# Kernel optimization log

Measured on AMD Instinct MI355X. Metric: run time of the kernel, lower is better.

The kernel has to match this reference:

```python
import jax, jax.numpy as jnp
import numpy as np

B, C, L, H, W = 2, 64, 8, 32, 32

def setup_inputs() -> dict:
    key = jax.random.key(0)
    ks = jax.random.split(key, 10)
    return {
        "q": jax.random.normal(ks[0], (B, C, L, H, W), dtype=jnp.float32),
        "k": jax.random.normal(ks[1], (B, C, L, H, W), dtype=jnp.float32),
        "v": jax.random.normal(ks[2], (B, C, L, H, W), dtype=jnp.float32),
        "wq": jax.random.normal(ks[3], (C,), dtype=jnp.float32) * 0.1,
        "bq": jax.random.normal(ks[4], (1,), dtype=jnp.float32) * 0.1,
        "wk": jax.random.normal(ks[5], (C,), dtype=jnp.float32) * 0.1,
        "bk": jax.random.normal(ks[6], (1,), dtype=jnp.float32) * 0.1,
        "wv": jax.random.normal(ks[7], (C, 3 * C), dtype=jnp.float32) * 0.1,
        "bv": jax.random.normal(ks[8], (C,), dtype=jnp.float32) * 0.1,
        "gamma_x": jax.random.normal(ks[9], (1,), dtype=jnp.float32) * 0.1,
    }


def reference(q, k, v, wq, bq, wk, bk, wv, bv, gamma_x):
    # q,k,v: [B,C,L,H,W]; 1x1x1 conv3d == channel contraction
    Bq, Cq, Lq, Hq, Wq = q.shape
    N = Lq * Hq * Wq
    qf = q.reshape(Bq, Cq, N)
    kf = k.reshape(Bq, Cq, N)
    vf = v.reshape(Bq, Cq, N)
    # query/key conv: C -> 1 channel => [B, N]
    pq = jnp.einsum('bcn,c->bn', qf, wq) + bq  # [B,N]
    pk = jnp.einsum('bcn,c->bn', kf, wk) + bk  # [B,N]
    # energy = bmm([B,N,1],[B,1,N]) = outer product -> [B,N,N]
    energy = pq[:, :, None] * pk[:, None, :]
    attn = jax.nn.softmax(energy, axis=-1)  # softmax over key index n
    # value path: cat(v, q, k) along channels -> [B,3C,N], then 3C -> C conv
    val = jnp.concatenate([vf, qf, kf], axis=1)
    pv = jnp.einsum('bdn,cd->bcn', val, wv) + bv[None, :, None]  # [B,C,N]
    # out[b,c,m] = sum_n pv[b,c,n] * attn[b,m,n]  (bmm with attn^T)
    out = jnp.einsum('bcn,bmn->bcm', pv, attn).reshape(Bq, Cq, Lq, Hq, Wq)
    return gamma_x * out + v
```

## Files before the change

### kernel.cpp

```cpp
#include <hip/hip_runtime.h>


typedef __attribute__((ext_vector_type(8))) __bf16 bf16x8;
typedef __attribute__((ext_vector_type(4))) float  f32x4;

#define NN 8192
#define CC 64
#define NJ 48

__global__ __launch_bounds__(256) void fused_kernel(
    const float* __restrict__ q, const float* __restrict__ k,
    const float* __restrict__ v,
    const float* __restrict__ wq, const float* __restrict__ bq,
    const float* __restrict__ wk, const float* __restrict__ bk,
    const float* __restrict__ wv, const float* __restrict__ bv,
    float* __restrict__ pq, float* __restrict__ G, float* __restrict__ T)
{
    __shared__ __align__(16) __bf16 val_sT[64][200];
    __shared__ __align__(16) __bf16 pv_s[64][72];
    __shared__ __align__(16) __bf16 V_s[NJ][72];
    __shared__ float pq4[4][64], pk4[4][64];

    int t = threadIdx.x, lane = t & 63, wid = t >> 6;
    int quad = lane >> 4, cl = lane & 15;
    int b  = blockIdx.x >> 7;
    int n0 = (blockIdx.x & 127) << 6;
    size_t bo = (size_t)b * CC * NN;

    bf16x8 wvA[6];
    const float* wr = wv + (size_t)(wid * 16 + cl) * 192;
    #pragma unroll
    for (int ks = 0; ks < 6; ks++) {
        f32x4 a0 = *(const f32x4*)(wr + ks * 32 + quad * 8);
        f32x4 a1 = *(const f32x4*)(wr + ks * 32 + quad * 8 + 4);
        #pragma unroll
        for (int e = 0; e < 4; e++) {
            wvA[ks][e]     = (__bf16)a0[e];
            wvA[ks][4 + e] = (__bf16)a1[e];
        }
    }
    float bvr[4];
    #pragma unroll
    for (int r = 0; r < 4; r++) bvr[r] = bv[wid * 16 + quad * 4 + r];

    {
        const float* qp = q + bo + (size_t)(wid * 16) * NN + n0 + lane;
        const float* kp = k + bo + (size_t)(wid * 16) * NN + n0 + lane;
        float aq = 0.f, ak = 0.f;
        #pragma unroll
        for (int d = 0; d < 16; d++) {
            aq = fmaf(qp[(size_t)d * NN], wq[wid * 16 + d], aq);
            ak = fmaf(kp[(size_t)d * NN], wk[wid * 16 + d], ak);
        }
        pq4[wid][lane] = aq;
        pk4[wid][lane] = ak;
    }

    float tile[8][8];
    int dt = 0, no = 0;
    if (wid > 0) {
        int idx = t - 64;
        dt = idx >> 3; no = idx & 7;
        int dbase = dt * 8;
        const float* src = (dbase < 64)  ? (v + bo + (size_t)dbase * NN)
                         : (dbase < 128) ? (q + bo + (size_t)(dbase - 64) * NN)
                                         : (k + bo + (size_t)(dbase - 128) * NN);
        #pragma unroll
        for (int dd = 0; dd < 8; dd++) {
            f32x4 x0 = *(const f32x4*)(src + (size_t)dd * NN + n0 + no * 8);
            f32x4 x1 = *(const f32x4*)(src + (size_t)dd * NN + n0 + no * 8 + 4);
            #pragma unroll
            for (int e = 0; e < 4; e++) { tile[dd][e] = x0[e]; tile[dd][4 + e] = x1[e]; }
        }
    }
    __syncthreads();

    if (wid == 0) {
        float pkv = pk4[0][lane] + pk4[1][lane] + pk4[2][lane] + pk4[3][lane] + bk[0];
        pq[b * NN + n0 + lane] =
            pq4[0][lane] + pq4[1][lane] + pq4[2][lane] + pq4[3][lane] + bq[0];
        float tp = 1.f;
        #pragma unroll
        for (int j = 0; j < NJ; j++) {
            V_s[j][lane] = (__bf16)tp;
            tp *= pkv;
        }
    } else {
        #pragma unroll
        for (int nn = 0; nn < 8; nn++) {
            bf16x8 wb;
            #pragma unroll
            for (int dd = 0; dd < 8; dd++) wb[dd] = (__bf16)tile[dd][nn];
            *(bf16x8*)&val_sT[no * 8 + nn][dt * 8] = wb;
        }
    }
    __syncthreads();

    f32x4 accP[4];
    #pragma unroll
    for (int nt = 0; nt < 4; nt++) accP[nt] = (f32x4){0.f, 0.f, 0.f, 0.f};
    #pragma unroll
    for (int ks = 0; ks < 6; ks++)
        #pragma unroll
        for (int nt = 0; nt < 4; nt++) {
            bf16x8 bfr = *(const bf16x8*)&val_sT[nt * 16 + cl][ks * 32 + quad * 8];
            accP[nt] = __builtin_amdgcn_mfma_f32_16x16x32_bf16(wvA[ks], bfr, accP[nt], 0, 0, 0);
        }

    #pragma unroll
    for (int nt = 0; nt < 4; nt++)
        #pragma unroll
        for (int r = 0; r < 4; r++)
            pv_s[wid * 16 + quad * 4 + r][nt * 16 + cl] = (__bf16)(accP[nt][r] + bvr[r]);

    f32x4 accG[3];
    #pragma unroll
    for (int jt = 0; jt < 3; jt++) accG[jt] = (f32x4){0.f, 0.f, 0.f, 0.f};
    #pragma unroll
    for (int k0 = 0; k0 < 64; k0 += 32) {
        bf16x8 a = *(const bf16x8*)&pv_s[wid * 16 + cl][k0 + quad * 8];
        #pragma unroll
        for (int jt = 0; jt < 3; jt++) {
            bf16x8 bfr = *(const bf16x8*)&V_s[jt * 16 + cl][k0 + quad * 8];
            accG[jt] = __builtin_amdgcn_mfma_f32_16x16x32_bf16(a, bfr, accG[jt], 0, 0, 0);
        }
    }

    #pragma unroll
    for (int jt = 0; jt < 3; jt++)
        #pragma unroll
        for (int r = 0; r < 4; r++)
            atomicAdd(&G[((size_t)b * CC + wid * 16 + quad * 4 + r) * NJ + jt * 16 + cl],
                      accG[jt][r]);

    if (t < NJ) {
        float tsum = 0.f;
        #pragma unroll
        for (int h = 0; h < 8; h++) {
            bf16x8 vv = *(const bf16x8*)&V_s[t][h * 8];
            #pragma unroll
            for (int e = 0; e < 8; e++) tsum += (float)vv[e];
        }
        atomicAdd(&T[b * NJ + t], tsum);
    }
}

__global__ __launch_bounds__(256) void eval_kernel(
    const float* __restrict__ pq, const float* __restrict__ G,
    const float* __restrict__ T, const float* __restrict__ v,
    const float* __restrict__ gamma, float* __restrict__ out)
{
    int t = threadIdx.x;
    int b   = blockIdx.x >> 8;
    int mch = (blockIdx.x >> 3) & 31;
    int cg  = blockIdx.x & 7;

    int m = mch * 256 + t;
    float s = pq[b * NN + m];
    const float* Gr = G + ((size_t)b * CC + cg * 8) * NJ;
    const float* Tr = T + b * NJ;

    float acc[8];
    #pragma unroll
    for (int c = 0; c < 8; c++) acc[c] = 0.f;
    float z = 0.f, cj = 1.f;
    #pragma unroll
    for (int j = 0; j < NJ; j++) {
        if (j > 0) cj *= s * (1.0f / (float)j);
        z = fmaf(cj, Tr[j], z);
        #pragma unroll
        for (int c = 0; c < 8; c++) acc[c] = fmaf(cj, Gr[c * NJ + j], acc[c]);
    }
    float gz = gamma[0] / z;

    #pragma unroll
    for (int c = 0; c < 8; c++) {
        size_t idx = ((size_t)b * CC + cg * 8 + c) * NN + m;
        out[idx] = fmaf(gz, acc[c], v[idx]);
    }
}

extern "C" void kernel_launch(void* const* d_in, const int* in_sizes, int n_in,
                              void* d_out, int out_size, void* d_ws, size_t ws_size,
                              hipStream_t stream)
{
    const float* q     = (const float*)d_in[0];
    const float* k     = (const float*)d_in[1];
    const float* v     = (const float*)d_in[2];
    const float* wq    = (const float*)d_in[3];
    const float* bq    = (const float*)d_in[4];
    const float* wk    = (const float*)d_in[5];
    const float* bk    = (const float*)d_in[6];
    const float* wv    = (const float*)d_in[7];
    const float* bv    = (const float*)d_in[8];
    const float* gamma = (const float*)d_in[9];

    float* pqw = (float*)d_ws;
    float* Gw  = pqw + 2 * NN;
    float* Tw  = Gw + 2 * CC * NJ;

    fused_kernel<<<256, 256, 0, stream>>>(q, k, v, wq, bq, wk, bk, wv, bv,
                                          pqw, Gw, Tw);
    eval_kernel<<<512, 256, 0, stream>>>(pqw, Gw, Tw, v, gamma, (float*)d_out);
}
```

Measured before the change: 92.60 us.

## Fuse projection and evaluation into one cooperative kernel with grid sync

Merges the accumulation kernel and the evaluation kernel into a single cooperative launch separated by a grid-wide barrier. The pq values stay in shared memory and each block evaluates outputs for its own 64 positions across all channels, which removes the second launch and the global round trip for pq. In exchange, the evaluation phase runs with fewer blocks and more serial work per thread, and it depends on cooperative launch support, falling back to the two-kernel path otherwise.

```diff
diff --git a/kernel.cpp b/kernel.cpp
--- a/kernel.cpp
+++ b/kernel.cpp
@@ -1,4 +1,7 @@
 #include <hip/hip_runtime.h>
+#include <hip/hip_cooperative_groups.h>
+
+namespace cg = cooperative_groups;
 
 
 typedef __attribute__((ext_vector_type(8))) __bf16 bf16x8;
@@ -7,6 +10,173 @@
 #define NN 8192
 #define CC 64
 #define NJ 48
+
+__global__ __launch_bounds__(256) void dam_coop(
+    const float* __restrict__ q, const float* __restrict__ k,
+    const float* __restrict__ v,
+    const float* __restrict__ wq, const float* __restrict__ bq,
+    const float* __restrict__ wk, const float* __restrict__ bk,
+    const float* __restrict__ wv, const float* __restrict__ bv,
+    const float* __restrict__ gamma, float* __restrict__ out,
+    float* __restrict__ G, float* __restrict__ T)
+{
+    __shared__ __align__(16) __bf16 val_sT[64][200];
+    __shared__ __align__(16) __bf16 pv_s[64][72];
+    __shared__ __align__(16) __bf16 V_s[NJ][72];
+    __shared__ float pq4[4][64], pk4[4][64];
+    __shared__ float pq_l[64];
+
+    int t = threadIdx.x, lane = t & 63, wid = t >> 6;
+    int quad = lane >> 4, cl = lane & 15;
+    int b  = blockIdx.x >> 7;
+    int n0 = (blockIdx.x & 127) << 6;
+    size_t bo = (size_t)b * CC * NN;
+
+    bf16x8 wvA[6];
+    const float* wr = wv + (size_t)(wid * 16 + cl) * 192;
+    #pragma unroll
+    for (int ks = 0; ks < 6; ks++) {
+        f32x4 a0 = *(const f32x4*)(wr + ks * 32 + quad * 8);
+        f32x4 a1 = *(const f32x4*)(wr + ks * 32 + quad * 8 + 4);
+        #pragma unroll
+        for (int e = 0; e < 4; e++) {
+            wvA[ks][e]     = (__bf16)a0[e];
+            wvA[ks][4 + e] = (__bf16)a1[e];
+        }
+    }
+    float bvr[4];
+    #pragma unroll
+    for (int r = 0; r < 4; r++) bvr[r] = bv[wid * 16 + quad * 4 + r];
+
+    {
+        const float* qp = q + bo + (size_t)(wid * 16) * NN + n0 + lane;
+        const float* kp = k + bo + (size_t)(wid * 16) * NN + n0 + lane;
+        float aq = 0.f, ak = 0.f;
+        #pragma unroll
+        for (int d = 0; d < 16; d++) {
+            aq = fmaf(qp[(size_t)d * NN], wq[wid * 16 + d], aq);
+            ak = fmaf(kp[(size_t)d * NN], wk[wid * 16 + d], ak);
+        }
+        pq4[wid][lane] = aq;
+        pk4[wid][lane] = ak;
+    }
+
+    float tile[8][8];
+    int dt = 0, no = 0;
+    if (wid > 0) {
+        int idx = t - 64;
+        dt = idx >> 3; no = idx & 7;
+        int dbase = dt * 8;
+        const float* src = (dbase < 64)  ? (v + bo + (size_t)dbase * NN)
+                         : (dbase < 128) ? (q + bo + (size_t)(dbase - 64) * NN)
+                                         : (k + bo + (size_t)(dbase - 128) * NN);
+        #pragma unroll
+        for (int dd = 0; dd < 8; dd++) {
+            f32x4 x0 = *(const f32x4*)(src + (size_t)dd * NN + n0 + no * 8);
+            f32x4 x1 = *(const f32x4*)(src + (size_t)dd * NN + n0 + no * 8 + 4);
+            #pragma unroll
+            for (int e = 0; e < 4; e++) { tile[dd][e] = x0[e]; tile[dd][4 + e] = x1[e]; }
+        }
+    }
+    __syncthreads();
+
+    if (wid == 0) {
+        float pkv = pk4[0][lane] + pk4[1][lane] + pk4[2][lane] + pk4[3][lane] + bk[0];
+        pq_l[lane] =
+            pq4[0][lane] + pq4[1][lane] + pq4[2][lane] + pq4[3][lane] + bq[0];
+        float tp = 1.f;
+        #pragma unroll
+        for (int j = 0; j < NJ; j++) {
+            V_s[j][lane] = (__bf16)tp;
+            tp *= pkv;
+        }
+    } else {
+        #pragma unroll
+        for (int nn = 0; nn < 8; nn++) {
+            bf16x8 wb;
+            #pragma unroll
+            for (int dd = 0; dd < 8; dd++) wb[dd] = (__bf16)tile[dd][nn];
+            *(bf16x8*)&val_sT[no * 8 + nn][dt * 8] = wb;
+        }
+    }
+    __syncthreads();
+
+    f32x4 accP[4];
+    #pragma unroll
+    for (int nt = 0; nt < 4; nt++) accP[nt] = (f32x4){0.f, 0.f, 0.f, 0.f};
+    #pragma unroll
+    for (int ks = 0; ks < 6; ks++)
+        #pragma unroll
+        for (int nt = 0; nt < 4; nt++) {
+            bf16x8 bfr = *(const bf16x8*)&val_sT[nt * 16 + cl][ks * 32 + quad * 8];
+            accP[nt] = __builtin_amdgcn_mfma_f32_16x16x32_bf16(wvA[ks], bfr, accP[nt], 0, 0, 0);
+        }
+
+    #pragma unroll
+    for (int nt = 0; nt < 4; nt++)
+        #pragma unroll
+        for (int r = 0; r < 4; r++)
+            pv_s[wid * 16 + quad * 4 + r][nt * 16 + cl] = (__bf16)(accP[nt][r] + bvr[r]);
+
+    f32x4 accG[3];
+    #pragma unroll
+    for (int jt = 0; jt < 3; jt++) accG[jt] = (f32x4){0.f, 0.f, 0.f, 0.f};
+    #pragma unroll
+    for (int k0 = 0; k0 < 64; k0 += 32) {
+        bf16x8 a = *(const bf16x8*)&pv_s[wid * 16 + cl][k0 + quad * 8];
+        #pragma unroll
+        for (int jt = 0; jt < 3; jt++) {
+            bf16x8 bfr = *(const bf16x8*)&V_s[jt * 16 + cl][k0 + quad * 8];
+            accG[jt] = __builtin_amdgcn_mfma_f32_16x16x32_bf16(a, bfr, accG[jt], 0, 0, 0);
+        }
+    }
+
+    #pragma unroll
+    for (int jt = 0; jt < 3; jt++)
+        #pragma unroll
+        for (int r = 0; r < 4; r++)
+            atomicAdd(&G[((size_t)b * CC + wid * 16 + quad * 4 + r) * NJ + jt * 16 + cl],
+                      accG[jt][r]);
+
+    if (t < NJ) {
+        float tsum = 0.f;
+        #pragma unroll
+        for (int h = 0; h < 8; h++) {
+            bf16x8 vv = *(const bf16x8*)&V_s[t][h * 8];
+            #pragma unroll
+            for (int e = 0; e < 8; e++) tsum += (float)vv[e];
+        }
+        atomicAdd(&T[b * NJ + t], tsum);
+    }
+
+    cg::this_grid().sync();
+
+    {
+        float s = pq_l[lane];
+        const float* Gr = G + ((size_t)b * CC + wid * 16) * NJ;
+        const float* Tr = T + b * NJ;
+
+        float cjv[NJ];
+        cjv[0] = 1.f;
+        float cj = 1.f;
+        #pragma unroll
+        for (int j = 1; j < NJ; j++) { cj *= s * (1.0f / (float)j); cjv[j] = cj; }
+
+        float z = 0.f;
+        #pragma unroll
+        for (int j = 0; j < NJ; j++) z = fmaf(cjv[j], Tr[j], z);
+        float gz = gamma[0] / z;
+
+        #pragma unroll
+        for (int i = 0; i < 16; i++) {
+            float a = 0.f;
+            #pragma unroll
+            for (int j = 0; j < NJ; j++) a = fmaf(cjv[j], Gr[i * NJ + j], a);
+            size_t idxo = ((size_t)b * CC + wid * 16 + i) * NN + n0 + lane;
+            out[idxo] = fmaf(gz, a, v[idxo]);
+        }
+    }
+}
 
 __global__ __launch_bounds__(256) void fused_kernel(
     const float* __restrict__ q, const float* __restrict__ k,
@@ -153,11 +323,11 @@
     int t = threadIdx.x;
     int b   = blockIdx.x >> 8;
     int mch = (blockIdx.x >> 3) & 31;
-    int cg  = blockIdx.x & 7;
+    int cg2 = blockIdx.x & 7;
 
     int m = mch * 256 + t;
     float s = pq[b * NN + m];
-    const float* Gr = G + ((size_t)b * CC + cg * 8) * NJ;
+    const float* Gr = G + ((size_t)b * CC + cg2 * 8) * NJ;
     const float* Tr = T + b * NJ;
 
     float acc[8];
@@ -175,7 +345,7 @@
 
     #pragma unroll
     for (int c = 0; c < 8; c++) {
-        size_t idx = ((size_t)b * CC + cg * 8 + c) * NN + m;
+        size_t idx = ((size_t)b * CC + cg2 * 8 + c) * NN + m;
         out[idx] = fmaf(gz, acc[c], v[idx]);
     }
 }
@@ -198,8 +368,19 @@
     float* pqw = (float*)d_ws;
     float* Gw  = pqw + 2 * NN;
     float* Tw  = Gw + 2 * CC * NJ;
-
-    fused_kernel<<<256, 256, 0, stream>>>(q, k, v, wq, bq, wk, bk, wv, bv,
-                                          pqw, Gw, Tw);
-    eval_kernel<<<512, 256, 0, stream>>>(pqw, Gw, Tw, v, gamma, (float*)d_out);
+    float* outp = (float*)d_out;
+
+    void* args[] = {
+        (void*)&q, (void*)&k, (void*)&v, (void*)&wq, (void*)&bq,
+        (void*)&wk, (void*)&bk, (void*)&wv, (void*)&bv, (void*)&gamma,
+        (void*)&outp, (void*)&Gw, (void*)&Tw
+    };
+    hipError_t err = hipLaunchCooperativeKernel(
+        (const void*)dam_coop, dim3(256), dim3(256), args, 0, stream);
+
+    if (err != hipSuccess) {
+        fused_kernel<<<256, 256, 0, stream>>>(q, k, v, wq, bq, wk, bk, wv, bv,
+                                              pqw, Gw, Tw);
+        eval_kernel<<<512, 256, 0, stream>>>(pqw, Gw, Tw, v, gamma, outp);
+    }
 }
```

Measured after the change: 137.6 us. +48.6%, slower.
